# Kernel tuning notes

Hardware: AMD Instinct MI355X
Metric: run time of the kernel (lower is better)

## Reference

```python
import jax, jax.numpy as jnp
import numpy as np

N, E, IN, H, C, T = 50000, 800000, 128, 64, 64, 2
F1, FO1 = H, H // T   # conv1: per-tower in/out feats
F2, FO2 = H, C // T   # conv2
STD_EPS = 1e-5
BN_EPS = 1e-5


def setup_inputs() -> dict:
    key = jax.random.key(0)
    ks = jax.random.split(key, 12)
    rn = lambda k, s, sc=0.05: jax.random.normal(k, s, jnp.float32) * sc
    return {
        "x": jax.random.normal(ks[0], (N, IN), jnp.float32),
        "embed_W": rn(ks[1], (IN, H)),
        "embed_b": jnp.zeros((H,), jnp.float32),
        "pre_W1": rn(ks[2], (T, 2 * F1, F1)),
        "pre_b1": jnp.zeros((T, F1), jnp.float32),
        "post_W1": rn(ks[3], (T, 13 * F1, FO1)),
        "post_b1": jnp.zeros((T, FO1), jnp.float32),
        "lin_W1": rn(ks[4], (H, H)),
        "lin_b1": jnp.zeros((H,), jnp.float32),
        "bn_gamma": jnp.ones((H,), jnp.float32),
        "bn_beta": jnp.zeros((H,), jnp.float32),
        "pre_W2": rn(ks[5], (T, 2 * F2, F2)),
        "pre_b2": jnp.zeros((T, F2), jnp.float32),
        "post_W2": rn(ks[6], (T, 13 * F2, FO2)),
        "post_b2": jnp.zeros((T, FO2), jnp.float32),
        "lin_W2": rn(ks[7], (C, C)),
        "lin_b2": jnp.zeros((C,), jnp.float32),
        "src": jax.random.randint(ks[8], (E,), 0, N, jnp.int32),
        "dst": jax.random.randint(ks[9], (E,), 0, N, jnp.int32),
    }


def _pna_conv(h, src, dst, deg_raw, degc, avg_log, preW, preb, postW, postb, linW, linb):
    # h: [N, F] node feats; messages flow src -> dst, aggregated at dst.
    m = jnp.concatenate([h[dst], h[src]], axis=-1)            # [E, 2F]  (cat[x_i, x_j])
    m = jnp.einsum('ef,tfg->etg', m, preW) + preb[None]       # [E, T, F] per-tower pre-NN
    seg = lambda v: jax.ops.segment_sum(v, dst, num_segments=N)
    cnt = degc[:, None, None]                                 # clamped degree >= 1
    has = (deg_raw > 0)[:, None, None]
    mean = seg(m) / cnt                                       # [N, T, F]
    mean_sq = seg(m * m) / cnt
    mn = jnp.where(has, jax.ops.segment_min(m, dst, num_segments=N), 0.0)
    mx = jnp.where(has, jax.ops.segment_max(m, dst, num_segments=N), 0.0)
    std = jnp.sqrt(jax.nn.relu(mean_sq - mean * mean) + STD_EPS)
    agg = jnp.concatenate([mean, mn, mx, std], axis=-1)       # [N, T, 4F]
    ld = jnp.log(degc + 1.0)[:, None, None]
    out = jnp.concatenate([agg, agg * (ld / avg_log), agg * (avg_log / ld)], axis=-1)  # [N, T, 12F]
    F = h.shape[-1]
    out = jnp.concatenate([jnp.broadcast_to(h[:, None, :], (N, T, F)), out], axis=-1)  # [N, T, 13F]
    out = jnp.einsum('ntf,tfg->ntg', out, postW) + postb[None]  # [N, T, FO] per-tower post-NN
    return out.reshape(N, -1) @ linW + linb                    # final mixing Linear(out, out)


def reference(x, embed_W, embed_b, pre_W1, pre_b1, post_W1, post_b1, lin_W1, lin_b1,
              bn_gamma, bn_beta, pre_W2, pre_b2, post_W2, post_b2, lin_W2, lin_b2,
              src, dst):
    deg_raw = jax.ops.segment_sum(jnp.ones((E,), jnp.float32), dst, num_segments=N)
    degc = jnp.maximum(deg_raw, 1.0)
    avg_log = jnp.mean(jnp.log(deg_raw + 1.0))  # avg_deg['log'] from the graph's degrees
    h = x @ embed_W + embed_b
    h = _pna_conv(h, src, dst, deg_raw, degc, avg_log,
                  pre_W1, pre_b1, post_W1, post_b1, lin_W1, lin_b1)
    mu = jnp.mean(h, axis=0)
    var = jnp.mean((h - mu) ** 2, axis=0)
    h = bn_gamma * (h - mu) / jnp.sqrt(var + BN_EPS) + bn_beta
    h = jax.nn.relu(h)  # dropout is identity in eval mode
    return _pna_conv(h, src, dst, deg_raw, degc, avg_log,
                     pre_W2, pre_b2, post_W2, post_b2, lin_W2, lin_b2)
```

## Files before the change

kernel.cpp:

```cpp
#include <hip/hip_runtime.h>

#define N_NODES 50000
#define E_EDGES 800000
#define IN_F    128
#define H_F     64
#define STD_EPS 1e-5f
#define BN_EPS  1e-5f

__global__ __launch_bounds__(256) void k_hist(const int* __restrict__ dst,
                                              int* __restrict__ deg) {
  int e = blockIdx.x * 256 + threadIdx.x;
  if (e < E_EDGES) atomicAdd(&deg[dst[e]], 1);
}

__global__ __launch_bounds__(256) void k_sumlog(const int* __restrict__ deg,
                                                float* __restrict__ scalars) {
  __shared__ float red[256];
  int i = blockIdx.x * 256 + threadIdx.x;
  float v = 0.f;
  if (i < N_NODES) v = logf((float)deg[i] + 1.0f);
  red[threadIdx.x] = v; __syncthreads();
  for (int s = 128; s > 0; s >>= 1) {
    if (threadIdx.x < s) red[threadIdx.x] += red[threadIdx.x + s];
    __syncthreads();
  }
  if (threadIdx.x == 0) atomicAdd(&scalars[0], red[0]);
}

__global__ __launch_bounds__(256) void k_scan_part(const int* __restrict__ deg,
                                                   int* __restrict__ partials) {
  __shared__ int red[256];
  int base = blockIdx.x * 1024;
  int s = 0;
  for (int j = threadIdx.x; j < 1024; j += 256) {
    int i = base + j;
    if (i < N_NODES) s += deg[i];
  }
  red[threadIdx.x] = s; __syncthreads();
  for (int st = 128; st > 0; st >>= 1) {
    if (threadIdx.x < st) red[threadIdx.x] += red[threadIdx.x + st];
    __syncthreads();
  }
  if (threadIdx.x == 0) partials[blockIdx.x] = red[0];
}

__global__ void k_scan_mid(int* __restrict__ partials, int nblk,
                           float* __restrict__ scalars) {
  if (threadIdx.x == 0) {
    int run = 0;
    for (int b = 0; b < nblk; b++) { int v = partials[b]; partials[b] = run; run += v; }
    scalars[1] = scalars[0] / (float)N_NODES;
  }
}

__global__ __launch_bounds__(256) void k_scan_final(const int* __restrict__ deg,
                                                    const int* __restrict__ partials,
                                                    int* __restrict__ row_ptr,
                                                    int* __restrict__ cursor) {
  __shared__ int ts[256];
  int base = blockIdx.x * 1024 + threadIdx.x * 4;
  int d[4]; int s = 0;
#pragma unroll
  for (int j = 0; j < 4; j++) {
    int i = base + j;
    d[j] = (i < N_NODES) ? deg[i] : 0;
    s += d[j];
  }
  ts[threadIdx.x] = s; __syncthreads();
  for (int off = 1; off < 256; off <<= 1) {
    int t = (threadIdx.x >= off) ? ts[threadIdx.x - off] : 0;
    __syncthreads();
    ts[threadIdx.x] += t;
    __syncthreads();
  }
  int excl = (threadIdx.x > 0) ? ts[threadIdx.x - 1] : 0;
  int run = partials[blockIdx.x] + excl;
#pragma unroll
  for (int j = 0; j < 4; j++) {
    int i = base + j;
    if (i < N_NODES) { row_ptr[i] = run; cursor[i] = run; run += d[j]; }
  }
  if (blockIdx.x == 0 && threadIdx.x == 0) row_ptr[N_NODES] = E_EDGES;
}

__global__ __launch_bounds__(256) void k_scatter(const int* __restrict__ src,
                                                 const int* __restrict__ dst,
                                                 int* __restrict__ cursor,
                                                 int* __restrict__ csr_src) {
  int e = blockIdx.x * 256 + threadIdx.x;
  if (e < E_EDGES) {
    int d = dst[e];
    int p = atomicAdd(&cursor[d], 1);
    csr_src[p] = src[e];
  }
}

__global__ __launch_bounds__(256) void k_embed(const float* __restrict__ x,
                                               const float* __restrict__ W,
                                               const float* __restrict__ bias,
                                               float* __restrict__ h) {
  __shared__ float sW[IN_F * 64];
  __shared__ float sx[IN_F * 20];
  for (int i = threadIdx.x; i < IN_F * 64; i += 256) sW[i] = W[i];
  int j = threadIdx.x & 63, ng = threadIdx.x >> 6;
  float bj = bias[j];
  for (int grp = blockIdx.x; grp < N_NODES / 16; grp += gridDim.x) {
    int n0 = grp * 16;
    __syncthreads();
    for (int idx = threadIdx.x; idx < 16 * IN_F; idx += 256) {
      int nl = idx >> 7, k = idx & 127;
      sx[k * 20 + nl] = x[(size_t)(n0 + nl) * IN_F + k];
    }
    __syncthreads();
    float a0 = bj, a1 = bj, a2 = bj, a3 = bj;
    const float* xp = &sx[ng * 4];
#pragma unroll 4
    for (int k = 0; k < IN_F; k++) {
      float4 xv = *(const float4*)&xp[k * 20];
      float w = sW[k * 64 + j];
      a0 = fmaf(xv.x, w, a0); a1 = fmaf(xv.y, w, a1);
      a2 = fmaf(xv.z, w, a2); a3 = fmaf(xv.w, w, a3);
    }
    size_t ob = (size_t)(n0 + ng * 4) * 64 + j;
    h[ob] = a0; h[ob + 64] = a1; h[ob + 128] = a2; h[ob + 192] = a3;
  }
}

template <bool BN>
__global__ __launch_bounds__(256) void k_preab(const float* __restrict__ hin,
                                               const float* __restrict__ preW,
                                               const float* __restrict__ preb,
                                               const float* __restrict__ bnscale,
                                               const float* __restrict__ bnshift,
                                               float* __restrict__ h2out,
                                               float* __restrict__ hA,
                                               float* __restrict__ hB) {
  __shared__ float sW[128 * 64];
  __shared__ float sh[64 * 20];
  int t = blockIdx.x & 1;
  const float* Wsrc = preW + (size_t)t * 128 * 64;
  for (int i = threadIdx.x; i < 128 * 64; i += 256) sW[i] = Wsrc[i];
  int f = threadIdx.x & 63, ng = threadIdx.x >> 6;
  float pb = preb[t * 64 + f];
  const float* wA = &sW[f];
  const float* wB = &sW[64 * 64 + f];
  int nblk2 = gridDim.x >> 1;
  for (int grp = blockIdx.x >> 1; grp < N_NODES / 16; grp += nblk2) {
    int n0 = grp * 16;
    __syncthreads();
    for (int idx = threadIdx.x; idx < 16 * 64; idx += 256) {
      int nl = idx >> 6, k = idx & 63;
      float v = hin[(size_t)(n0 + nl) * 64 + k];
      if (BN) {
        v = fmaxf(fmaf(v, bnscale[k], bnshift[k]), 0.f);
        if (t == 0) h2out[(size_t)(n0 + nl) * 64 + k] = v;
      }
      sh[k * 20 + nl] = v;
    }
    __syncthreads();
    float a0 = pb, a1 = pb, a2 = pb, a3 = pb;
    float b0 = 0, b1 = 0, b2 = 0, b3 = 0;
    const float* hp = &sh[ng * 4];
#pragma unroll 4
    for (int k = 0; k < 64; k++) {
      float4 hv = *(const float4*)&hp[k * 20];
      float wa = wA[k * 64], wb = wB[k * 64];
      a0 = fmaf(hv.x, wa, a0); a1 = fmaf(hv.y, wa, a1);
      a2 = fmaf(hv.z, wa, a2); a3 = fmaf(hv.w, wa, a3);
      b0 = fmaf(hv.x, wb, b0); b1 = fmaf(hv.y, wb, b1);
      b2 = fmaf(hv.z, wb, b2); b3 = fmaf(hv.w, wb, b3);
    }
    size_t nb = (size_t)(n0 + ng * 4);
    int tf = t * 64 + f;
    hA[nb * 128 + tf] = a0;          hB[nb * 128 + tf] = b0;
    hA[(nb + 1) * 128 + tf] = a1;    hB[(nb + 1) * 128 + tf] = b1;
    hA[(nb + 2) * 128 + tf] = a2;    hB[(nb + 2) * 128 + tf] = b2;
    hA[(nb + 3) * 128 + tf] = a3;    hB[(nb + 3) * 128 + tf] = b3;
  }
}

__global__ __launch_bounds__(256, 6) void k_conv(const float* __restrict__ hA,
                                                 const float* __restrict__ hB,
                                                 const float* __restrict__ hskip,
                                                 const int* __restrict__ row_ptr,
                                                 const int* __restrict__ csr_src,
                                                 const float* __restrict__ postW,
                                                 const float* __restrict__ postb,
                                                 const float* __restrict__ linW,
                                                 const float* __restrict__ linb,
                                                 const float* __restrict__ scalars,
                                                 float* __restrict__ out) {
  __shared__ float smem[2 * 13 * 4 * 64];
  int w = threadIdx.x >> 6, lane = threadIdx.x & 63;
  int n = blockIdx.x * 4 + w;
  int t = lane >> 5, fb = (lane & 31) * 2;
  int off = t * 64 + fb;

  float2 a = *(const float2*)&hA[(size_t)n * 128 + off];
  int rp0 = __builtin_amdgcn_readfirstlane(row_ptr[n]);
  int rp1 = __builtin_amdgcn_readfirstlane(row_ptr[n + 1]);
  float sx0=0,sy0=0,qx0=0,qy0=0, sx1=0,sy1=0,qx1=0,qy1=0;
  float mnx0=INFINITY,mny0=INFINITY,mxx0=-INFINITY,mxy0=-INFINITY;
  float mnx1=INFINITY,mny1=INFINITY,mxx1=-INFINITY,mxy1=-INFINITY;
  int i = rp0;
  int end4 = rp0 + ((rp1 - rp0) & ~3);
  if (i < end4) {
    int s0 = csr_src[i], s1 = csr_src[i+1], s2 = csr_src[i+2], s3 = csr_src[i+3];
    while (true) {
      float2 v0 = *(const float2*)&hB[(size_t)s0 * 128 + off];
      float2 v1 = *(const float2*)&hB[(size_t)s1 * 128 + off];
      float2 v2 = *(const float2*)&hB[(size_t)s2 * 128 + off];
      float2 v3 = *(const float2*)&hB[(size_t)s3 * 128 + off];
      i += 4;
      bool more = (i < end4);
      if (more) { s0 = csr_src[i]; s1 = csr_src[i+1]; s2 = csr_src[i+2]; s3 = csr_src[i+3]; }
      float e0x = v0.x + a.x, e0y = v0.y + a.y;
      float e1x = v1.x + a.x, e1y = v1.y + a.y;
      float e2x = v2.x + a.x, e2y = v2.y + a.y;
      float e3x = v3.x + a.x, e3y = v3.y + a.y;
      sx0 += e0x; qx0 = fmaf(e0x,e0x,qx0); mnx0 = fminf(mnx0,e0x); mxx0 = fmaxf(mxx0,e0x);
      sy0 += e0y; qy0 = fmaf(e0y,e0y,qy0); mny0 = fminf(mny0,e0y); mxy0 = fmaxf(mxy0,e0y);
      sx1 += e1x; qx1 = fmaf(e1x,e1x,qx1); mnx1 = fminf(mnx1,e1x); mxx1 = fmaxf(mxx1,e1x);
      sy1 += e1y; qy1 = fmaf(e1y,e1y,qy1); mny1 = fminf(mny1,e1y); mxy1 = fmaxf(mxy1,e1y);
      sx0 += e2x; qx0 = fmaf(e2x,e2x,qx0); mnx0 = fminf(mnx0,e2x); mxx0 = fmaxf(mxx0,e2x);
      sy0 += e2y; qy0 = fmaf(e2y,e2y,qy0); mny0 = fminf(mny0,e2y); mxy0 = fmaxf(mxy0,e2y);
      sx1 += e3x; qx1 = fmaf(e3x,e3x,qx1); mnx1 = fminf(mnx1,e3x); mxx1 = fmaxf(mxx1,e3x);
      sy1 += e3y; qy1 = fmaf(e3y,e3y,qy1); mny1 = fminf(mny1,e3y); mxy1 = fmaxf(mxy1,e3y);
      if (!more) break;
    }
  }
  {
    int r = rp1 - i;
    if (r > 0) {
      int e1i = (r > 1) ? i + 1 : i;
      int e2i = (r > 2) ? i + 2 : i;
      int t0 = csr_src[i], t1 = csr_src[e1i], t2 = csr_src[e2i];
      float2 u0 = *(const float2*)&hB[(size_t)t0 * 128 + off];
      float2 u1 = *(const float2*)&hB[(size_t)t1 * 128 + off];
      float2 u2 = *(const float2*)&hB[(size_t)t2 * 128 + off];
      float ex = u0.x + a.x, ey = u0.y + a.y;
      sx0 += ex; qx0 = fmaf(ex,ex,qx0); mnx0 = fminf(mnx0,ex); mxx0 = fmaxf(mxx0,ex);
      sy0 += ey; qy0 = fmaf(ey,ey,qy0); mny0 = fminf(mny0,ey); mxy0 = fmaxf(mxy0,ey);
      if (r > 1) {
        ex = u1.x + a.x; ey = u1.y + a.y;
        sx1 += ex; qx1 = fmaf(ex,ex,qx1); mnx1 = fminf(mnx1,ex); mxx1 = fmaxf(mxx1,ex);
        sy1 += ey; qy1 = fmaf(ey,ey,qy1); mny1 = fminf(mny1,ey); mxy1 = fmaxf(mxy1,ey);
      }
      if (r > 2) {
        ex = u2.x + a.x; ey = u2.y + a.y;
        sx0 += ex; qx0 = fmaf(ex,ex,qx0); mnx0 = fminf(mnx0,ex); mxx0 = fmaxf(mxx0,ex);
        sy0 += ey; qy0 = fmaf(ey,ey,qy0); mny0 = fminf(mny0,ey); mxy0 = fmaxf(mxy0,ey);
      }
    }
  }
  int dg = rp1 - rp0;
  float cnt = (float)(dg > 0 ? dg : 1);
  float inv = 1.0f / cnt;
  float meanx = (sx0 + sx1) * inv, meany = (sy0 + sy1) * inv;
  float qx = qx0 + qx1, qy = qy0 + qy1;
  float sdx = sqrtf(fmaxf(qx * inv - meanx * meanx, 0.f) + STD_EPS);
  float sdy = sqrtf(fmaxf(qy * inv - meany * meany, 0.f) + STD_EPS);
  float mnx = fminf(mnx0, mnx1), mny = fminf(mny0, mny1);
  float mxx = fmaxf(mxx0, mxx1), mxy = fmaxf(mxy0, mxy1);
  if (dg == 0) { mnx = 0; mny = 0; mxx = 0; mxy = 0; }
  float avg = scalars[1];
  float ldv = logf(cnt + 1.f);
  float sA = ldv / avg, sB = avg / ldv;
  float2 hsv = *(const float2*)&hskip[(size_t)n * 64 + fb];

  {
    float* bp = &smem[t * (13 * 256) + w * 64 + fb];
    *(float2*)&bp[0]        = make_float2(hsv.x, hsv.y);
    *(float2*)&bp[256]      = make_float2(meanx, meany);
    *(float2*)&bp[2 * 256]  = make_float2(mnx, mny);
    *(float2*)&bp[3 * 256]  = make_float2(mxx, mxy);
    *(float2*)&bp[4 * 256]  = make_float2(sdx, sdy);
    *(float2*)&bp[5 * 256]  = make_float2(meanx * sA, meany * sA);
    *(float2*)&bp[6 * 256]  = make_float2(mnx * sA, mny * sA);
    *(float2*)&bp[7 * 256]  = make_float2(mxx * sA, mxy * sA);
    *(float2*)&bp[8 * 256]  = make_float2(sdx * sA, sdy * sA);
    *(float2*)&bp[9 * 256]  = make_float2(meanx * sB, meany * sB);
    *(float2*)&bp[10 * 256] = make_float2(mnx * sB, mny * sB);
    *(float2*)&bp[11 * 256] = make_float2(mxx * sB, mxy * sB);
    *(float2*)&bp[12 * 256] = make_float2(sdx * sB, sdy * sB);
  }
  __syncthreads();

  float c0 = 0, c1 = 0, c2 = 0, c3 = 0;
  {
    int tC = lane >> 5, g = lane & 31, hf0 = w * 16;
    const float* pwt = &postW[(size_t)tC * (832 * 32) + g];
#pragma unroll
    for (int feat = 0; feat < 13; feat++) {
      const float* lp = &smem[(tC * 13 + feat) * 256 + hf0];
      const float* pw = pwt + (size_t)(feat * 64 + hf0) * 32;
#pragma unroll
      for (int j = 0; j < 16; j += 4) {
        float w0 = pw[j * 32], w1 = pw[j * 32 + 32], w2 = pw[j * 32 + 64], w3 = pw[j * 32 + 96];
        float4 v0 = *(const float4*)(lp + j);
        float4 v1 = *(const float4*)(lp + 64 + j);
        float4 v2 = *(const float4*)(lp + 128 + j);
        float4 v3 = *(const float4*)(lp + 192 + j);
        c0 = fmaf(v0.w, w3, fmaf(v0.z, w2, fmaf(v0.y, w1, fmaf(v0.x, w0, c0))));
        c1 = fmaf(v1.w, w3, fmaf(v1.z, w2, fmaf(v1.y, w1, fmaf(v1.x, w0, c1))));
        c2 = fmaf(v2.w, w3, fmaf(v2.z, w2, fmaf(v2.y, w1, fmaf(v2.x, w0, c2))));
        c3 = fmaf(v3.w, w3, fmaf(v3.z, w2, fmaf(v3.y, w1, fmaf(v3.x, w0, c3))));
      }
    }
  }
  __syncthreads();

  {
    int sw = (w + (lane >> 3)) & 3;
    smem[((0 * 64 + lane) << 2) + sw] = c0;
    smem[((1 * 64 + lane) << 2) + sw] = c1;
    smem[((2 * 64 + lane) << 2) + sw] = c2;
    smem[((3 * 64 + lane) << 2) + sw] = c3;
  }
  __syncthreads();

  {
    float4 p = *(const float4*)&smem[(w * 64 + lane) << 2];
    float po = p.x + p.y + p.z + p.w + postb[lane];
    smem[1024 + w * 64 + lane] = po;
  }
  __syncthreads();

  {
    float acc = linb[lane];
    const float* lw = linW + lane;
    const float* pov = &smem[1024 + w * 64];
#pragma unroll
    for (int i2 = 0; i2 < 64; i2 += 4) {
      float4 p = *(const float4*)&pov[i2];
      acc = fmaf(p.x, lw[i2 * 64], acc);
      acc = fmaf(p.y, lw[(i2 + 1) * 64], acc);
      acc = fmaf(p.z, lw[(i2 + 2) * 64], acc);
      acc = fmaf(p.w, lw[(i2 + 3) * 64], acc);
    }
    out[(size_t)n * 64 + lane] = acc;
  }
}

__global__ __launch_bounds__(256) void k_bnstats(const float* __restrict__ y,
                                                 float* __restrict__ bnsum,
                                                 float* __restrict__ bnsumsq) {
  __shared__ float r1[256], r2[256];
  int c = threadIdx.x & 63, r = threadIdx.x >> 6;
  float s = 0, q = 0;
  for (int n = blockIdx.x * 4 + r; n < N_NODES; n += gridDim.x * 4) {
    float v = y[(size_t)n * 64 + c];
    s += v; q = fmaf(v, v, q);
  }
  r1[threadIdx.x] = s; r2[threadIdx.x] = q; __syncthreads();
  if (threadIdx.x < 64) {
    s = r1[threadIdx.x] + r1[threadIdx.x + 64] + r1[threadIdx.x + 128] + r1[threadIdx.x + 192];
    q = r2[threadIdx.x] + r2[threadIdx.x + 64] + r2[threadIdx.x + 128] + r2[threadIdx.x + 192];
    atomicAdd(&bnsum[threadIdx.x], s);
    atomicAdd(&bnsumsq[threadIdx.x], q);
  }
}

__global__ void k_bnfin(const float* __restrict__ bnsum, const float* __restrict__ bnsumsq,
                        const float* __restrict__ gamma, const float* __restrict__ beta,
                        float* __restrict__ bnscale, float* __restrict__ bnshift) {
  int c = threadIdx.x;
  if (c < 64) {
    float mu = bnsum[c] * (1.f / N_NODES);
    float var = bnsumsq[c] * (1.f / N_NODES) - mu * mu;
    float sc = gamma[c] / sqrtf(var + BN_EPS);
    bnscale[c] = sc;
    bnshift[c] = fmaf(-mu, sc, beta[c]);
  }
}

extern "C" void kernel_launch(void* const* d_in, const int* in_sizes, int n_in,
                              void* d_out, int out_size, void* d_ws, size_t ws_size,
                              hipStream_t stream) {
  const float* x      = (const float*)d_in[0];
  const float* embW   = (const float*)d_in[1];
  const float* embB   = (const float*)d_in[2];
  const float* preW1  = (const float*)d_in[3];
  const float* preb1  = (const float*)d_in[4];
  const float* postW1 = (const float*)d_in[5];
  const float* postb1 = (const float*)d_in[6];
  const float* linW1  = (const float*)d_in[7];
  const float* linb1  = (const float*)d_in[8];
  const float* gamma  = (const float*)d_in[9];
  const float* beta   = (const float*)d_in[10];
  const float* preW2  = (const float*)d_in[11];
  const float* preb2  = (const float*)d_in[12];
  const float* postW2 = (const float*)d_in[13];
  const float* postb2 = (const float*)d_in[14];
  const float* linW2  = (const float*)d_in[15];
  const float* linb2  = (const float*)d_in[16];
  const int*   src    = (const int*)d_in[17];
  const int*   dst    = (const int*)d_in[18];
  float* out = (float*)d_out;

  char* w = (char*)d_ws;
  size_t o = 0;
  int*   deg     = (int*)(w + o);   o += (size_t)N_NODES * 4;
  float* scalars = (float*)(w + o); o += 64;
  float* bnsum   = (float*)(w + o); o += 256;
  float* bnsumsq = (float*)(w + o); o += 256;
  float* bnscale = (float*)(w + o); o += 256;
  float* bnshift = (float*)(w + o); o += 256;
  size_t zero_len = o;
  o = (o + 255) & ~(size_t)255;
  int* partials = (int*)(w + o);  o += 256;
  int* row_ptr  = (int*)(w + o);  o += (size_t)(N_NODES + 1) * 4; o = (o + 255) & ~(size_t)255;
  int* cursor   = (int*)(w + o);  o += (size_t)N_NODES * 4;       o = (o + 255) & ~(size_t)255;
  int* csr      = (int*)(w + o);  o += (size_t)E_EDGES * 4;       o = (o + 255) & ~(size_t)255;
  float* h1 = (float*)(w + o); o += (size_t)N_NODES * 64 * 4;
  float* y1 = (float*)(w + o); o += (size_t)N_NODES * 64 * 4;
  float* h2 = (float*)(w + o); o += (size_t)N_NODES * 64 * 4;
  float* hA = (float*)(w + o); o += (size_t)N_NODES * 128 * 4;
  float* hB = (float*)(w + o); o += (size_t)N_NODES * 128 * 4;

  hipMemsetAsync(w, 0, zero_len, stream);

  const int NBLK_SCAN = (N_NODES + 1023) / 1024;
  k_hist<<<(E_EDGES + 255) / 256, 256, 0, stream>>>(dst, deg);
  k_sumlog<<<(N_NODES + 255) / 256, 256, 0, stream>>>(deg, scalars);
  k_scan_part<<<NBLK_SCAN, 256, 0, stream>>>(deg, partials);
  k_scan_mid<<<1, 64, 0, stream>>>(partials, NBLK_SCAN, scalars);
  k_scan_final<<<NBLK_SCAN, 256, 0, stream>>>(deg, partials, row_ptr, cursor);
  k_scatter<<<(E_EDGES + 255) / 256, 256, 0, stream>>>(src, dst, cursor, csr);

  k_embed<<<768, 256, 0, stream>>>(x, embW, embB, h1);

  k_preab<false><<<1024, 256, 0, stream>>>(h1, preW1, preb1, nullptr, nullptr, nullptr, hA, hB);
  k_conv<<<N_NODES / 4, 256, 0, stream>>>(hA, hB, h1, row_ptr, csr,
                                          postW1, postb1, linW1, linb1, scalars, y1);
  k_bnstats<<<256, 256, 0, stream>>>(y1, bnsum, bnsumsq);
  k_bnfin<<<1, 64, 0, stream>>>(bnsum, bnsumsq, gamma, beta, bnscale, bnshift);

  k_preab<true><<<1024, 256, 0, stream>>>(y1, preW2, preb2, bnscale, bnshift, h2, hA, hB);
  k_conv<<<N_NODES / 4, 256, 0, stream>>>(hA, hB, h2, row_ptr, csr,
                                          postW2, postb2, linW2, linb2, scalars, out);
}
```

Before: 647.4 us.

## Factor degree scalers out of post-NN and process 8 nodes per block

The conv kernel now handles 8 nodes per block, two per wave. Instead of materialising the 13 scaled feature groups, it keeps 5 groups in shared memory and accumulates three partial products (identity, amplification, attenuation), combining them with per-node scalars at the end. Post-NN and final linear weights are transposed once per call so each thread reads contiguous float4 weight vectors. Per-node weight traffic and FMAs in the post-NN are cut, at the cost of more registers (launch bound lowered to 5) and fewer blocks.

```diff
diff --git a/kernel.cpp b/kernel.cpp
--- a/kernel.cpp
+++ b/kernel.cpp
@@ -92,6 +92,29 @@
     int d = dst[e];
     int p = atomicAdd(&cursor[d], 1);
     csr_src[p] = src[e];
+  }
+}
+
+__global__ __launch_bounds__(256) void k_transpose(const float* __restrict__ pW1,
+                                                   const float* __restrict__ pW2,
+                                                   const float* __restrict__ lW1,
+                                                   const float* __restrict__ lW2,
+                                                   float* __restrict__ pWT,
+                                                   float* __restrict__ lWT) {
+  int idx = blockIdx.x * 256 + threadIdx.x;
+  if (idx < 106496) {
+    int layer = idx / 53248, r = idx % 53248;
+    int t = r / 26624, r2 = r % 26624;
+    int f = r2 / 32, g = r2 % 32;
+    const float* srcp = layer ? pW2 : pW1;
+    pWT[(size_t)layer * 53248 + (size_t)(t * 32 + g) * 832 + f] =
+        srcp[(size_t)t * 26624 + f * 32 + g];
+  } else if (idx < 114688) {
+    int j = idx - 106496;
+    int layer = j / 4096, r2 = j % 4096;
+    int row = r2 / 64, c = r2 % 64;
+    const float* srcl = layer ? lW2 : lW1;
+    lWT[(size_t)layer * 4096 + c * 64 + row] = srcl[row * 64 + c];
   }
 }
 
@@ -179,166 +202,183 @@
   }
 }
 
-__global__ __launch_bounds__(256, 6) void k_conv(const float* __restrict__ hA,
+__global__ __launch_bounds__(256, 5) void k_conv(const float* __restrict__ hA,
                                                  const float* __restrict__ hB,
                                                  const float* __restrict__ hskip,
                                                  const int* __restrict__ row_ptr,
                                                  const int* __restrict__ csr_src,
-                                                 const float* __restrict__ postW,
+                                                 const float* __restrict__ postWT,
                                                  const float* __restrict__ postb,
-                                                 const float* __restrict__ linW,
+                                                 const float* __restrict__ linWT,
                                                  const float* __restrict__ linb,
                                                  const float* __restrict__ scalars,
                                                  float* __restrict__ out) {
-  __shared__ float smem[2 * 13 * 4 * 64];
+  __shared__ float sm[2 * 5 * 8 * 64];
+  __shared__ float sAB[16];
   int w = threadIdx.x >> 6, lane = threadIdx.x & 63;
-  int n = blockIdx.x * 4 + w;
+  int n0 = blockIdx.x * 8;
   int t = lane >> 5, fb = (lane & 31) * 2;
   int off = t * 64 + fb;
-
-  float2 a = *(const float2*)&hA[(size_t)n * 128 + off];
-  int rp0 = __builtin_amdgcn_readfirstlane(row_ptr[n]);
-  int rp1 = __builtin_amdgcn_readfirstlane(row_ptr[n + 1]);
-  float sx0=0,sy0=0,qx0=0,qy0=0, sx1=0,sy1=0,qx1=0,qy1=0;
-  float mnx0=INFINITY,mny0=INFINITY,mxx0=-INFINITY,mxy0=-INFINITY;
-  float mnx1=INFINITY,mny1=INFINITY,mxx1=-INFINITY,mxy1=-INFINITY;
-  int i = rp0;
-  int end4 = rp0 + ((rp1 - rp0) & ~3);
-  if (i < end4) {
-    int s0 = csr_src[i], s1 = csr_src[i+1], s2 = csr_src[i+2], s3 = csr_src[i+3];
-    while (true) {
-      float2 v0 = *(const float2*)&hB[(size_t)s0 * 128 + off];
-      float2 v1 = *(const float2*)&hB[(size_t)s1 * 128 + off];
-      float2 v2 = *(const float2*)&hB[(size_t)s2 * 128 + off];
-      float2 v3 = *(const float2*)&hB[(size_t)s3 * 128 + off];
-      i += 4;
-      bool more = (i < end4);
-      if (more) { s0 = csr_src[i]; s1 = csr_src[i+1]; s2 = csr_src[i+2]; s3 = csr_src[i+3]; }
-      float e0x = v0.x + a.x, e0y = v0.y + a.y;
-      float e1x = v1.x + a.x, e1y = v1.y + a.y;
-      float e2x = v2.x + a.x, e2y = v2.y + a.y;
-      float e3x = v3.x + a.x, e3y = v3.y + a.y;
-      sx0 += e0x; qx0 = fmaf(e0x,e0x,qx0); mnx0 = fminf(mnx0,e0x); mxx0 = fmaxf(mxx0,e0x);
-      sy0 += e0y; qy0 = fmaf(e0y,e0y,qy0); mny0 = fminf(mny0,e0y); mxy0 = fmaxf(mxy0,e0y);
-      sx1 += e1x; qx1 = fmaf(e1x,e1x,qx1); mnx1 = fminf(mnx1,e1x); mxx1 = fmaxf(mxx1,e1x);
-      sy1 += e1y; qy1 = fmaf(e1y,e1y,qy1); mny1 = fminf(mny1,e1y); mxy1 = fmaxf(mxy1,e1y);
-      sx0 += e2x; qx0 = fmaf(e2x,e2x,qx0); mnx0 = fminf(mnx0,e2x); mxx0 = fmaxf(mxx0,e2x);
-      sy0 += e2y; qy0 = fmaf(e2y,e2y,qy0); mny0 = fminf(mny0,e2y); mxy0 = fmaxf(mxy0,e2y);
-      sx1 += e3x; qx1 = fmaf(e3x,e3x,qx1); mnx1 = fminf(mnx1,e3x); mxx1 = fmaxf(mxx1,e3x);
-      sy1 += e3y; qy1 = fmaf(e3y,e3y,qy1); mny1 = fminf(mny1,e3y); mxy1 = fmaxf(mxy1,e3y);
-      if (!more) break;
-    }
-  }
-  {
-    int r = rp1 - i;
-    if (r > 0) {
-      int e1i = (r > 1) ? i + 1 : i;
-      int e2i = (r > 2) ? i + 2 : i;
-      int t0 = csr_src[i], t1 = csr_src[e1i], t2 = csr_src[e2i];
-      float2 u0 = *(const float2*)&hB[(size_t)t0 * 128 + off];
-      float2 u1 = *(const float2*)&hB[(size_t)t1 * 128 + off];
-      float2 u2 = *(const float2*)&hB[(size_t)t2 * 128 + off];
-      float ex = u0.x + a.x, ey = u0.y + a.y;
-      sx0 += ex; qx0 = fmaf(ex,ex,qx0); mnx0 = fminf(mnx0,ex); mxx0 = fmaxf(mxx0,ex);
-      sy0 += ey; qy0 = fmaf(ey,ey,qy0); mny0 = fminf(mny0,ey); mxy0 = fmaxf(mxy0,ey);
-      if (r > 1) {
-        ex = u1.x + a.x; ey = u1.y + a.y;
-        sx1 += ex; qx1 = fmaf(ex,ex,qx1); mnx1 = fminf(mnx1,ex); mxx1 = fmaxf(mxx1,ex);
-        sy1 += ey; qy1 = fmaf(ey,ey,qy1); mny1 = fminf(mny1,ey); mxy1 = fmaxf(mxy1,ey);
+  float avg = scalars[1];
+
+#pragma unroll 1
+  for (int k = 0; k < 2; k++) {
+    int nl = w * 2 + k;
+    int n = n0 + nl;
+    float2 a = *(const float2*)&hA[(size_t)n * 128 + off];
+    int rp0 = __builtin_amdgcn_readfirstlane(row_ptr[n]);
+    int rp1 = __builtin_amdgcn_readfirstlane(row_ptr[n + 1]);
+    float sx0=0,sy0=0,qx0=0,qy0=0, sx1=0,sy1=0,qx1=0,qy1=0;
+    float mnx0=INFINITY,mny0=INFINITY,mxx0=-INFINITY,mxy0=-INFINITY;
+    float mnx1=INFINITY,mny1=INFINITY,mxx1=-INFINITY,mxy1=-INFINITY;
+    int i = rp0;
+    int end4 = rp0 + ((rp1 - rp0) & ~3);
+    if (i < end4) {
+      int s0 = csr_src[i], s1 = csr_src[i+1], s2 = csr_src[i+2], s3 = csr_src[i+3];
+      while (true) {
+        float2 v0 = *(const float2*)&hB[(size_t)s0 * 128 + off];
+        float2 v1 = *(const float2*)&hB[(size_t)s1 * 128 + off];
+        float2 v2 = *(const float2*)&hB[(size_t)s2 * 128 + off];
+        float2 v3 = *(const float2*)&hB[(size_t)s3 * 128 + off];
+        i += 4;
+        bool more = (i < end4);
+        if (more) { s0 = csr_src[i]; s1 = csr_src[i+1]; s2 = csr_src[i+2]; s3 = csr_src[i+3]; }
+        float e0x = v0.x + a.x, e0y = v0.y + a.y;
+        float e1x = v1.x + a.x, e1y = v1.y + a.y;
+        float e2x = v2.x + a.x, e2y = v2.y + a.y;
+        float e3x = v3.x + a.x, e3y = v3.y + a.y;
+        sx0 += e0x; qx0 = fmaf(e0x,e0x,qx0); mnx0 = fminf(mnx0,e0x); mxx0 = fmaxf(mxx0,e0x);
+        sy0 += e0y; qy0 = fmaf(e0y,e0y,qy0); mny0 = fminf(mny0,e0y); mxy0 = fmaxf(mxy0,e0y);
+        sx1 += e1x; qx1 = fmaf(e1x,e1x,qx1); mnx1 = fminf(mnx1,e1x); mxx1 = fmaxf(mxx1,e1x);
+        sy1 += e1y; qy1 = fmaf(e1y,e1y,qy1); mny1 = fminf(mny1,e1y); mxy1 = fmaxf(mxy1,e1y);
+        sx0 += e2x; qx0 = fmaf(e2x,e2x,qx0); mnx0 = fminf(mnx0,e2x); mxx0 = fmaxf(mxx0,e2x);
+        sy0 += e2y; qy0 = fmaf(e2y,e2y,qy0); mny0 = fminf(mny0,e2y); mxy0 = fmaxf(mxy0,e2y);
+        sx1 += e3x; qx1 = fmaf(e3x,e3x,qx1); mnx1 = fminf(mnx1,e3x); mxx1 = fmaxf(mxx1,e3x);
+        sy1 += e3y; qy1 = fmaf(e3y,e3y,qy1); mny1 = fminf(mny1,e3y); mxy1 = fmaxf(mxy1,e3y);
+        if (!more) break;
       }
-      if (r > 2) {
-        ex = u2.x + a.x; ey = u2.y + a.y;
+    }
+    {
+      int r = rp1 - i;
+      if (r > 0) {
+        int e1i = (r > 1) ? i + 1 : i;
+        int e2i = (r > 2) ? i + 2 : i;
+        int t0 = csr_src[i], t1 = csr_src[e1i], t2 = csr_src[e2i];
+        float2 u0 = *(const float2*)&hB[(size_t)t0 * 128 + off];
+        float2 u1 = *(const float2*)&hB[(size_t)t1 * 128 + off];
+        float2 u2 = *(const float2*)&hB[(size_t)t2 * 128 + off];
+        float ex = u0.x + a.x, ey = u0.y + a.y;
         sx0 += ex; qx0 = fmaf(ex,ex,qx0); mnx0 = fminf(mnx0,ex); mxx0 = fmaxf(mxx0,ex);
         sy0 += ey; qy0 = fmaf(ey,ey,qy0); mny0 = fminf(mny0,ey); mxy0 = fmaxf(mxy0,ey);
+        if (r > 1) {
+          ex = u1.x + a.x; ey = u1.y + a.y;
+          sx1 += ex; qx1 = fmaf(ex,ex,qx1); mnx1 = fminf(mnx1,ex); mxx1 = fmaxf(mxx1,ex);
+          sy1 += ey; qy1 = fmaf(ey,ey,qy1); mny1 = fminf(mny1,ey); mxy1 = fmaxf(mxy1,ey);
+        }
+        if (r > 2) {
+          ex = u2.x + a.x; ey = u2.y + a.y;
+          sx0 += ex; qx0 = fmaf(ex,ex,qx0); mnx0 = fminf(mnx0,ex); mxx0 = fmaxf(mxx0,ex);
+          sy0 += ey; qy0 = fmaf(ey,ey,qy0); mny0 = fminf(mny0,ey); mxy0 = fmaxf(mxy0,ey);
+        }
       }
     }
-  }
-  int dg = rp1 - rp0;
-  float cnt = (float)(dg > 0 ? dg : 1);
-  float inv = 1.0f / cnt;
-  float meanx = (sx0 + sx1) * inv, meany = (sy0 + sy1) * inv;
-  float qx = qx0 + qx1, qy = qy0 + qy1;
-  float sdx = sqrtf(fmaxf(qx * inv - meanx * meanx, 0.f) + STD_EPS);
-  float sdy = sqrtf(fmaxf(qy * inv - meany * meany, 0.f) + STD_EPS);
-  float mnx = fminf(mnx0, mnx1), mny = fminf(mny0, mny1);
-  float mxx = fmaxf(mxx0, mxx1), mxy = fmaxf(mxy0, mxy1);
-  if (dg == 0) { mnx = 0; mny = 0; mxx = 0; mxy = 0; }
-  float avg = scalars[1];
-  float ldv = logf(cnt + 1.f);
-  float sA = ldv / avg, sB = avg / ldv;
-  float2 hsv = *(const float2*)&hskip[(size_t)n * 64 + fb];
-
+    int dg = rp1 - rp0;
+    float cnt = (float)(dg > 0 ? dg : 1);
+    float inv = 1.0f / cnt;
+    float meanx = (sx0 + sx1) * inv, meany = (sy0 + sy1) * inv;
+    float qx = qx0 + qx1, qy = qy0 + qy1;
+    float sdx = sqrtf(fmaxf(qx * inv - meanx * meanx, 0.f) + STD_EPS);
+    float sdy = sqrtf(fmaxf(qy * inv - meany * meany, 0.f) + STD_EPS);
+    float mnx = fminf(mnx0, mnx1), mny = fminf(mny0, mny1);
+    float mxx = fmaxf(mxx0, mxx1), mxy = fmaxf(mxy0, mxy1);
+    if (dg == 0) { mnx = 0; mny = 0; mxx = 0; mxy = 0; }
+    float ldv = logf(cnt + 1.f);
+    float2 hsv = *(const float2*)&hskip[(size_t)n * 64 + fb];
+    float* bp = &sm[t * 2560 + nl * 64 + fb];
+    *(float2*)&bp[0]    = hsv;
+    *(float2*)&bp[512]  = make_float2(meanx, meany);
+    *(float2*)&bp[1024] = make_float2(mnx, mny);
+    *(float2*)&bp[1536] = make_float2(mxx, mxy);
+    *(float2*)&bp[2048] = make_float2(sdx, sdy);
+    if (lane == 0) { sAB[nl] = ldv / avg; sAB[8 + nl] = avg / ldv; }
+  }
+  __syncthreads();
+
+  float g1[8] = {0,0,0,0,0,0,0,0};
+  float g2[8] = {0,0,0,0,0,0,0,0};
+  float g3[8] = {0,0,0,0,0,0,0,0};
   {
-    float* bp = &smem[t * (13 * 256) + w * 64 + fb];
-    *(float2*)&bp[0]        = make_float2(hsv.x, hsv.y);
-    *(float2*)&bp[256]      = make_float2(meanx, meany);
-    *(float2*)&bp[2 * 256]  = make_float2(mnx, mny);
-    *(float2*)&bp[3 * 256]  = make_float2(mxx, mxy);
-    *(float2*)&bp[4 * 256]  = make_float2(sdx, sdy);
-    *(float2*)&bp[5 * 256]  = make_float2(meanx * sA, meany * sA);
-    *(float2*)&bp[6 * 256]  = make_float2(mnx * sA, mny * sA);
-    *(float2*)&bp[7 * 256]  = make_float2(mxx * sA, mxy * sA);
-    *(float2*)&bp[8 * 256]  = make_float2(sdx * sA, sdy * sA);
-    *(float2*)&bp[9 * 256]  = make_float2(meanx * sB, meany * sB);
-    *(float2*)&bp[10 * 256] = make_float2(mnx * sB, mny * sB);
-    *(float2*)&bp[11 * 256] = make_float2(mxx * sB, mxy * sB);
-    *(float2*)&bp[12 * 256] = make_float2(sdx * sB, sdy * sB);
-  }
+    int g = lane & 31, hf0 = w * 16;
+    const float* wbase = &postWT[(size_t)(t * 32 + g) * 832 + hf0];
+    const float* vb = &sm[t * 2560 + hf0];
+#pragma unroll
+    for (int j = 0; j < 16; j += 4) {
+      float4 wh = *(const float4*)&wbase[j];
+#pragma unroll
+      for (int nn = 0; nn < 8; nn++) {
+        float4 v = *(const float4*)&vb[nn * 64 + j];
+        g1[nn] = fmaf(v.w, wh.w, fmaf(v.z, wh.z, fmaf(v.y, wh.y, fmaf(v.x, wh.x, g1[nn]))));
+      }
+    }
+#pragma unroll
+    for (int fa = 0; fa < 4; fa++) {
+#pragma unroll
+      for (int j = 0; j < 16; j += 4) {
+        int o = 64 + fa * 64 + j;
+        float4 w1 = *(const float4*)&wbase[o];
+        float4 w2 = *(const float4*)&wbase[o + 256];
+        float4 w3 = *(const float4*)&wbase[o + 512];
+        const float* vfa = &vb[(1 + fa) * 512 + j];
+#pragma unroll
+        for (int nn = 0; nn < 8; nn++) {
+          float4 v = *(const float4*)&vfa[nn * 64];
+          g1[nn] = fmaf(v.w, w1.w, fmaf(v.z, w1.z, fmaf(v.y, w1.y, fmaf(v.x, w1.x, g1[nn]))));
+          g2[nn] = fmaf(v.w, w2.w, fmaf(v.z, w2.z, fmaf(v.y, w2.y, fmaf(v.x, w2.x, g2[nn]))));
+          g3[nn] = fmaf(v.w, w3.w, fmaf(v.z, w3.z, fmaf(v.y, w3.y, fmaf(v.x, w3.x, g3[nn]))));
+        }
+      }
+    }
+  }
+  float o8[8];
+#pragma unroll
+  for (int nn = 0; nn < 8; nn++)
+    o8[nn] = fmaf(sAB[8 + nn], g3[nn], fmaf(sAB[nn], g2[nn], g1[nn]));
   __syncthreads();
 
-  float c0 = 0, c1 = 0, c2 = 0, c3 = 0;
   {
-    int tC = lane >> 5, g = lane & 31, hf0 = w * 16;
-    const float* pwt = &postW[(size_t)tC * (832 * 32) + g];
-#pragma unroll
-    for (int feat = 0; feat < 13; feat++) {
-      const float* lp = &smem[(tC * 13 + feat) * 256 + hf0];
-      const float* pw = pwt + (size_t)(feat * 64 + hf0) * 32;
-#pragma unroll
-      for (int j = 0; j < 16; j += 4) {
-        float w0 = pw[j * 32], w1 = pw[j * 32 + 32], w2 = pw[j * 32 + 64], w3 = pw[j * 32 + 96];
-        float4 v0 = *(const float4*)(lp + j);
-        float4 v1 = *(const float4*)(lp + 64 + j);
-        float4 v2 = *(const float4*)(lp + 128 + j);
-        float4 v3 = *(const float4*)(lp + 192 + j);
-        c0 = fmaf(v0.w, w3, fmaf(v0.z, w2, fmaf(v0.y, w1, fmaf(v0.x, w0, c0))));
-        c1 = fmaf(v1.w, w3, fmaf(v1.z, w2, fmaf(v1.y, w1, fmaf(v1.x, w0, c1))));
-        c2 = fmaf(v2.w, w3, fmaf(v2.z, w2, fmaf(v2.y, w1, fmaf(v2.x, w0, c2))));
-        c3 = fmaf(v3.w, w3, fmaf(v3.z, w2, fmaf(v3.y, w1, fmaf(v3.x, w0, c3))));
-      }
-    }
+    int sw = (w + (lane >> 4)) & 3;
+#pragma unroll
+    for (int nn = 0; nn < 8; nn++)
+      sm[((nn * 64 + lane) << 2) + sw] = o8[nn];
   }
   __syncthreads();
 
   {
-    int sw = (w + (lane >> 3)) & 3;
-    smem[((0 * 64 + lane) << 2) + sw] = c0;
-    smem[((1 * 64 + lane) << 2) + sw] = c1;
-    smem[((2 * 64 + lane) << 2) + sw] = c2;
-    smem[((3 * 64 + lane) << 2) + sw] = c3;
+#pragma unroll
+    for (int r = 0; r < 2; r++) {
+      int idx = r * 256 + (int)threadIdx.x;
+      float4 p = *(const float4*)&sm[idx << 2];
+      sm[2048 + idx] = p.x + p.y + p.z + p.w + postb[idx & 63];
+    }
   }
   __syncthreads();
 
   {
-    float4 p = *(const float4*)&smem[(w * 64 + lane) << 2];
-    float po = p.x + p.y + p.z + p.w + postb[lane];
-    smem[1024 + w * 64 + lane] = po;
-  }
-  __syncthreads();
-
-  {
-    float acc = linb[lane];
-    const float* lw = linW + lane;
-    const float* pov = &smem[1024 + w * 64];
-#pragma unroll
-    for (int i2 = 0; i2 < 64; i2 += 4) {
-      float4 p = *(const float4*)&pov[i2];
-      acc = fmaf(p.x, lw[i2 * 64], acc);
-      acc = fmaf(p.y, lw[(i2 + 1) * 64], acc);
-      acc = fmaf(p.z, lw[(i2 + 2) * 64], acc);
-      acc = fmaf(p.w, lw[(i2 + 3) * 64], acc);
-    }
-    out[(size_t)n * 64 + lane] = acc;
+    float acc0 = linb[lane], acc1 = acc0;
+    const float* lwt = &linWT[(size_t)lane * 64];
+    const float* p0 = &sm[2048 + (w * 2) * 64];
+    const float* p1 = p0 + 64;
+#pragma unroll
+    for (int c = 0; c < 64; c += 4) {
+      float4 lw = *(const float4*)&lwt[c];
+      float4 pa = *(const float4*)&p0[c];
+      float4 pb2 = *(const float4*)&p1[c];
+      acc0 = fmaf(pa.w, lw.w, fmaf(pa.z, lw.z, fmaf(pa.y, lw.y, fmaf(pa.x, lw.x, acc0))));
+      acc1 = fmaf(pb2.w, lw.w, fmaf(pb2.z, lw.z, fmaf(pb2.y, lw.y, fmaf(pb2.x, lw.x, acc1))));
+    }
+    size_t ob = (size_t)(n0 + w * 2) * 64 + lane;
+    out[ob] = acc0;
+    out[ob + 64] = acc1;
   }
 }
 
@@ -412,6 +452,8 @@
   int* row_ptr  = (int*)(w + o);  o += (size_t)(N_NODES + 1) * 4; o = (o + 255) & ~(size_t)255;
   int* cursor   = (int*)(w + o);  o += (size_t)N_NODES * 4;       o = (o + 255) & ~(size_t)255;
   int* csr      = (int*)(w + o);  o += (size_t)E_EDGES * 4;       o = (o + 255) & ~(size_t)255;
+  float* postWT = (float*)(w + o); o += (size_t)2 * 53248 * 4;
+  float* linWT  = (float*)(w + o); o += (size_t)2 * 4096 * 4;
   float* h1 = (float*)(w + o); o += (size_t)N_NODES * 64 * 4;
   float* y1 = (float*)(w + o); o += (size_t)N_NODES * 64 * 4;
   float* h2 = (float*)(w + o); o += (size_t)N_NODES * 64 * 4;
@@ -427,16 +469,18 @@
   k_scan_mid<<<1, 64, 0, stream>>>(partials, NBLK_SCAN, scalars);
   k_scan_final<<<NBLK_SCAN, 256, 0, stream>>>(deg, partials, row_ptr, cursor);
   k_scatter<<<(E_EDGES + 255) / 256, 256, 0, stream>>>(src, dst, cursor, csr);
+  k_transpose<<<448, 256, 0, stream>>>(postW1, postW2, linW1, linW2, postWT, linWT);
 
   k_embed<<<768, 256, 0, stream>>>(x, embW, embB, h1);
 
   k_preab<false><<<1024, 256, 0, stream>>>(h1, preW1, preb1, nullptr, nullptr, nullptr, hA, hB);
-  k_conv<<<N_NODES / 4, 256, 0, stream>>>(hA, hB, h1, row_ptr, csr,
-                                          postW1, postb1, linW1, linb1, scalars, y1);
+  k_conv<<<N_NODES / 8, 256, 0, stream>>>(hA, hB, h1, row_ptr, csr,
+                                          postWT, postb1, linWT, linb1, scalars, y1);
   k_bnstats<<<256, 256, 0, stream>>>(y1, bnsum, bnsumsq);
   k_bnfin<<<1, 64, 0, stream>>>(bnsum, bnsumsq, gamma, beta, bnscale, bnshift);
 
   k_preab<true><<<1024, 256, 0, stream>>>(y1, preW2, preb2, bnscale, bnshift, h2, hA, hB);
-  k_conv<<<N_NODES / 4, 256, 0, stream>>>(hA, hB, h2, row_ptr, csr,
-                                          postW2, postb2, linW2, linb2, scalars, out);
-}
+  k_conv<<<N_NODES / 8, 256, 0, stream>>>(hA, hB, h2, row_ptr, csr,
+                                          postWT + 53248, postb2, linWT + 4096, linb2,
+                                          scalars, out);
+}
```

After: 1.003 ms. +54.9%, slower.
